# Kernel tuning notes

Measured on AMD Instinct MI355X. Metric: run time of the kernel, lower is better.

## Reference

```python
import jax, jax.numpy as jnp
import numpy as np

B, N, D, S, H, ITERS = 128, 4096, 64, 7, 128, 3
EPS = 1e-8
LN_EPS = 1e-5


def _ln(x, g, b):
    mu = jnp.mean(x, axis=-1, keepdims=True)
    var = jnp.mean(jnp.square(x - mu), axis=-1, keepdims=True)
    return (x - mu) * jax.lax.rsqrt(var + LN_EPS) * g + b


def setup_inputs() -> dict:
    key = jax.random.key(0)
    ks = jax.random.split(key, 20)
    xav = lambda k, shp: jax.random.normal(k, shp, jnp.float32) * (2.0 / sum(shp[-2:])) ** 0.5
    inp = {
        "inputs": jax.random.normal(ks[0], (B, N, D), jnp.float32),
        "noise_bg": jax.random.normal(ks[1], (B, 1, D), jnp.float32),
        "noise_fg": jax.random.normal(ks[2], (B, S - 1, D), jnp.float32),
        "ln_in_g": jnp.ones((D,), jnp.float32), "ln_in_b": jnp.zeros((D,), jnp.float32),
        "ln_slot_g": jnp.ones((D,), jnp.float32), "ln_slot_b": jnp.zeros((D,), jnp.float32),
        "ln_mlp_g": jnp.ones((D,), jnp.float32), "ln_mlp_b": jnp.zeros((D,), jnp.float32),
        "Wq": xav(ks[3], (D, D)), "Wk": xav(ks[4], (D, D)), "Wv": xav(ks[5], (D, D)),
        "W_ih": xav(ks[6], (3 * D, D)), "W_hh": xav(ks[7], (3 * D, D)),
        "b_ih": jnp.zeros((3 * D,), jnp.float32), "b_hh": jnp.zeros((3 * D,), jnp.float32),
        "mlp_w1": xav(ks[8], (H, D)), "mlp_b1": jnp.zeros((H,), jnp.float32),
        "mlp_w2": xav(ks[9], (D, H)), "mlp_b2": jnp.zeros((D,), jnp.float32),
        "slots_bg_mu": xav(ks[10], (1, 1, D)),
        "slots_bg_log_sigma": xav(ks[11], (1, 1, D)),
        "slots_mu": xav(ks[12], (1, 1, D)),
        "slots_log_sigma": xav(ks[13], (1, 1, D)),
    }
    return inp


def _gru(x, h, W_ih, W_hh, b_ih, b_hh):
    # x, h: [M, D]; PyTorch GRUCell math, gate order r, z, n
    gi = x @ W_ih.T + b_ih
    gh = h @ W_hh.T + b_hh
    i_r, i_z, i_n = jnp.split(gi, 3, axis=-1)
    h_r, h_z, h_n = jnp.split(gh, 3, axis=-1)
    r = jax.nn.sigmoid(i_r + h_r)
    z = jax.nn.sigmoid(i_z + h_z)
    n = jnp.tanh(i_n + r * h_n)
    return (1.0 - z) * n + z * h


def reference(inputs, noise_bg, noise_fg, ln_in_g, ln_in_b, ln_slot_g, ln_slot_b,
              ln_mlp_g, ln_mlp_b, Wq, Wk, Wv, W_ih, W_hh, b_ih, b_hh,
              mlp_w1, mlp_b1, mlp_w2, mlp_b2,
              slots_bg_mu, slots_bg_log_sigma, slots_mu, slots_log_sigma):
    x = _ln(inputs, ln_in_g, ln_in_b)          # [B, N, D]
    k = jnp.einsum('bnd,ed->bne', x, Wk)       # [B, N, D]
    v = jnp.einsum('bnd,ed->bne', x, Wv)

    bg = slots_bg_mu + jnp.exp(slots_bg_log_sigma) * noise_bg   # [B, 1, D]
    fg = slots_mu + jnp.exp(slots_log_sigma) * noise_fg          # [B, S-1, D]
    slots = jnp.concatenate([bg, fg], axis=1)                    # [B, S, D]

    scale = D ** (-0.5)
    for _ in range(ITERS):
        slots_prev = slots
        s = _ln(slots, ln_slot_g, ln_slot_b)
        q = jnp.einsum('bsd,ed->bse', s, Wq)                     # [B, S, D]
        logits = scale * jnp.einsum('bnd,bsd->bns', k, q)        # [B, N, S]
        attn = jax.nn.softmax(logits, axis=-1) + EPS             # softmax over slots
        attn = attn / jnp.sum(attn, axis=1, keepdims=True)       # renorm over inputs
        updates = jnp.einsum('bns,bnd->bsd', attn, v)            # [B, S, D]
        h = _gru(updates.reshape(B * S, D), slots_prev.reshape(B * S, D),
                 W_ih, W_hh, b_ih, b_hh).reshape(B, S, D)
        m = _ln(h, ln_mlp_g, ln_mlp_b)
        m = jax.nn.relu(m @ mlp_w1.T + mlp_b1) @ mlp_w2.T + mlp_b2
        slots = h + m
    return slots
```

## Files before the change

kernel.cpp:

```cpp
#include <hip/hip_runtime.h>

#define BB 128
#define NN 4096
#define DD 64
#define SS 7
#define HH 128
#define N_ITERS 3
#define EPS_ATTN 1e-8f
#define LN_EPS 1e-5f

typedef unsigned short ushortT;
using short8  = __attribute__((ext_vector_type(8))) short;
using floatx4 = __attribute__((ext_vector_type(4))) float;
using uint4v  = __attribute__((ext_vector_type(4))) unsigned;

__device__ __forceinline__ ushortT f2bf(float f) {
    unsigned x = __builtin_bit_cast(unsigned, f);
    x = x + 0x7fff + ((x >> 16) & 1);
    return (ushortT)(x >> 16);
}
__device__ __forceinline__ void wave_stats64(float x, float& mu, float& var) {
    float s1 = x, s2 = x * x;
#pragma unroll
    for (int off = 32; off > 0; off >>= 1) {
        s1 += __shfl_xor(s1, off);
        s2 += __shfl_xor(s2, off);
    }
    mu  = s1 * (1.f / 64.f);
    var = s2 * (1.f / 64.f) - mu * mu;
}

__global__ void prep_w(const float* __restrict__ Wih, const float* __restrict__ Whh,
                       const float* __restrict__ w1, const float* __restrict__ w2,
                       const float* __restrict__ Wv, const float* __restrict__ Wq,
                       const float* __restrict__ Wk,
                       float* __restrict__ WihT, float* __restrict__ WhhT,
                       float* __restrict__ w1T, float* __restrict__ w2T,
                       float* __restrict__ WvT, float* __restrict__ WqkT) {
    if (blockIdx.x >= 192) {
        int idx = (blockIdx.x - 192) * 256 + threadIdx.x;
        int d = idx >> 6, tt = idx & 63;
        float acc = 0.f;
#pragma unroll 8
        for (int e = 0; e < 64; ++e) acc += Wk[e * 64 + tt] * Wq[e * 64 + d];
        WqkT[d * 64 + tt] = 0.125f * acc;
        return;
    }
    int i = blockIdx.x * 256 + threadIdx.x;
    if (i < 12288) {
        int e = i >> 6, d = i & 63;
        WihT[d * 192 + e] = Wih[i];
    } else if (i < 24576) {
        int j = i - 12288; int e = j >> 6, d = j & 63;
        WhhT[d * 192 + e] = Whh[j];
    } else if (i < 32768) {
        int j = i - 24576; int e = j >> 6, d = j & 63;
        w1T[d * 128 + e] = w1[j];
    } else if (i < 40960) {
        int j = i - 32768; int e = j >> 7, h = j & 127;
        w2T[h * 64 + e] = w2[j];
    } else if (i < 45056) {
        int j = i - 40960; int d = j >> 6, e = j & 63;
        WvT[e * 64 + d] = Wv[j];
    }
}

__global__ __launch_bounds__(256) void attn_kernel(
    int first,
    const float* __restrict__ x,
    const float* __restrict__ lng, const float* __restrict__ lnb,
    ushortT* __restrict__ xnf,
    const ushortT* __restrict__ qk_bf,
    float* __restrict__ pxn_p, float* __restrict__ den_p) {
    int t = threadIdx.x;
    int ck = blockIdx.x, b = ck >> 5;
    int w = t >> 6, lane = t & 63, m = lane & 15, qd = lane >> 4;
    __shared__ __align__(16) ushortT xnT[64 * 140];
    __shared__ __align__(16) ushortT p_lds[16][136];

    short8 aq0 = {}, aq1 = {};
    if (m < 8) {
        const ushortT* qb = qk_bf + b * 512 + m * 64 + qd * 8;
        aq0 = *reinterpret_cast<const short8*>(qb);
        aq1 = *reinterpret_cast<const short8*>(qb + 32);
    }

    unsigned xw[2][8];
    if (first) {
        float4 g4[2][2], b4[2][2];
#pragma unroll
        for (int c = 0; c < 2; ++c) {
            g4[c][0] = *reinterpret_cast<const float4*>(lng + c * 32 + qd * 8);
            g4[c][1] = *reinterpret_cast<const float4*>(lng + c * 32 + qd * 8 + 4);
            b4[c][0] = *reinterpret_cast<const float4*>(lnb + c * 32 + qd * 8);
            b4[c][1] = *reinterpret_cast<const float4*>(lnb + c * 32 + qd * 8 + 4);
        }
#pragma unroll
        for (int tile = 0; tile < 2; ++tile) {
            long R = (long)ck * 128 + w * 32 + tile * 16 + m;
            float4 xa[2][2];
#pragma unroll
            for (int c = 0; c < 2; ++c) {
                xa[c][0] = *reinterpret_cast<const float4*>(x + R * 64 + c * 32 + qd * 8);
                xa[c][1] = *reinterpret_cast<const float4*>(x + R * 64 + c * 32 + qd * 8 + 4);
            }
            float s1 = 0.f, s2 = 0.f;
#pragma unroll
            for (int c = 0; c < 2; ++c)
#pragma unroll
                for (int h = 0; h < 2; ++h) {
                    float4 v = xa[c][h];
                    s1 += v.x + v.y + v.z + v.w;
                    s2 += v.x * v.x + v.y * v.y + v.z * v.z + v.w * v.w;
                }
            s1 += __shfl_xor(s1, 16); s2 += __shfl_xor(s2, 16);
            s1 += __shfl_xor(s1, 32); s2 += __shfl_xor(s2, 32);
            float mu = s1 * (1.f / 64.f);
            float var = s2 * (1.f / 64.f) - mu * mu;
            float rs = rsqrtf(var + LN_EPS);
#pragma unroll
            for (int c = 0; c < 2; ++c)
#pragma unroll
                for (int h = 0; h < 2; ++h) {
                    float n0 = (xa[c][h].x - mu) * rs * g4[c][h].x + b4[c][h].x;
                    float n1 = (xa[c][h].y - mu) * rs * g4[c][h].y + b4[c][h].y;
                    float n2 = (xa[c][h].z - mu) * rs * g4[c][h].z + b4[c][h].z;
                    float n3 = (xa[c][h].w - mu) * rs * g4[c][h].w + b4[c][h].w;
                    xw[tile][c * 4 + h * 2]     = (unsigned)f2bf(n0) | ((unsigned)f2bf(n1) << 16);
                    xw[tile][c * 4 + h * 2 + 1] = (unsigned)f2bf(n2) | ((unsigned)f2bf(n3) << 16);
                }
            ushortT* xp = xnf + (long)ck * 8192 + w * 2048 + tile * 1024 + lane * 16;
            *reinterpret_cast<uint4*>(xp) =
                make_uint4(xw[tile][0], xw[tile][1], xw[tile][2], xw[tile][3]);
            *reinterpret_cast<uint4*>(xp + 8) =
                make_uint4(xw[tile][4], xw[tile][5], xw[tile][6], xw[tile][7]);
        }
    } else {
#pragma unroll
        for (int tile = 0; tile < 2; ++tile) {
            const ushortT* xp = xnf + (long)ck * 8192 + w * 2048 + tile * 1024 + lane * 16;
            uint4 u0 = *reinterpret_cast<const uint4*>(xp);
            uint4 u1 = *reinterpret_cast<const uint4*>(xp + 8);
            xw[tile][0] = u0.x; xw[tile][1] = u0.y; xw[tile][2] = u0.z; xw[tile][3] = u0.w;
            xw[tile][4] = u1.x; xw[tile][5] = u1.y; xw[tile][6] = u1.z; xw[tile][7] = u1.w;
        }
    }

#pragma unroll
    for (int tile = 0; tile < 2; ++tile) {
        int Re = (w * 32 + tile * 16 + m) & ~1;
#pragma unroll
        for (int c = 0; c < 2; ++c) {
            unsigned pt[4];
#pragma unroll
            for (int k = 0; k < 4; ++k) pt[k] = __shfl_xor(xw[tile][c * 4 + k], 1);
#pragma unroll
            for (int kk = 0; kk < 2; ++kk) {
                unsigned own = (m & 1) ? xw[tile][c * 4 + 2 + kk] : xw[tile][c * 4 + kk];
                unsigned par = (m & 1) ? pt[2 + kk] : pt[kk];
                unsigned a   = (m & 1) ? par : own;
                unsigned bb  = (m & 1) ? own : par;
                unsigned lo = (a & 0xffffu) | (bb << 16);
                unsigned hi = (a >> 16)     | (bb & 0xffff0000u);
                int e = c * 32 + qd * 8 + 2 * kk + ((m & 1) ? 4 : 0);
                *reinterpret_cast<unsigned*>(&xnT[e * 140 + Re])       = lo;
                *reinterpret_cast<unsigned*>(&xnT[(e + 1) * 140 + Re]) = hi;
            }
        }
    }

    floatx4 accT0 = {0.f, 0.f, 0.f, 0.f}, accT1 = {0.f, 0.f, 0.f, 0.f};
    {
        uint4v b00 = {xw[0][0], xw[0][1], xw[0][2], xw[0][3]};
        uint4v b01 = {xw[0][4], xw[0][5], xw[0][6], xw[0][7]};
        accT0 = __builtin_amdgcn_mfma_f32_16x16x32_bf16(aq0,
                    __builtin_bit_cast(short8, b00), accT0, 0, 0, 0);
        accT0 = __builtin_amdgcn_mfma_f32_16x16x32_bf16(aq1,
                    __builtin_bit_cast(short8, b01), accT0, 0, 0, 0);
        uint4v b10 = {xw[1][0], xw[1][1], xw[1][2], xw[1][3]};
        uint4v b11 = {xw[1][4], xw[1][5], xw[1][6], xw[1][7]};
        accT1 = __builtin_amdgcn_mfma_f32_16x16x32_bf16(aq0,
                    __builtin_bit_cast(short8, b10), accT1, 0, 0, 0);
        accT1 = __builtin_amdgcn_mfma_f32_16x16x32_bf16(aq1,
                    __builtin_bit_cast(short8, b11), accT1, 0, 0, 0);
    }

    float lgA[4], lgB[4];
#pragma unroll
    for (int r = 0; r < 4; ++r) {
        float hi = __shfl_xor(accT1[r], 32);
        float wk = (qd < 2) ? accT0[r] : hi;
        float pr = __shfl_xor(wk, 16);
        lgA[r] = (qd & 1) ? pr : wk;
        lgB[r] = (qd & 1) ? wk : pr;
    }
    float mx = fmaxf(fmaxf(fmaxf(lgA[0], lgA[1]), fmaxf(lgA[2], lgA[3])),
                     fmaxf(fmaxf(lgB[0], lgB[1]), lgB[2]));
    float eA[4], eB[3], sum = 0.f;
#pragma unroll
    for (int r = 0; r < 4; ++r) { eA[r] = __expf(lgA[r] - mx); sum += eA[r]; }
#pragma unroll
    for (int r = 0; r < 3; ++r) { eB[r] = __expf(lgB[r] - mx); sum += eB[r]; }
    float inv = 1.f / sum;
    int prow = w * 32 + (qd >> 1) * 16 + m;
    if ((qd & 1) == 0) {
#pragma unroll
        for (int r = 0; r < 4; ++r) p_lds[r][prow] = f2bf(eA[r] * inv + EPS_ATTN);
    } else {
#pragma unroll
        for (int r = 0; r < 3; ++r) p_lds[4 + r][prow] = f2bf(eB[r] * inv + EPS_ATTN);
    }
    __syncthreads();

    short8 ones;
#pragma unroll
    for (int j = 0; j < 8; ++j) ones[j] = (short)0x3F80;

    floatx4 acc2 = {0.f, 0.f, 0.f, 0.f}, accd = {0.f, 0.f, 0.f, 0.f};
#pragma unroll
    for (int ks = 0; ks < 4; ++ks) {
        short8 ap = *reinterpret_cast<const short8*>(&p_lds[m][ks * 32 + qd * 8]);
        const ushortT* xp = xnT + (w * 16 + m) * 140 + ks * 32 + qd * 8;
        uint2 u0 = *reinterpret_cast<const uint2*>(xp);
        uint2 u1 = *reinterpret_cast<const uint2*>(xp + 4);
        uint4v bb = {u0.x, u0.y, u1.x, u1.y};
        acc2 = __builtin_amdgcn_mfma_f32_16x16x32_bf16(ap,
                   __builtin_bit_cast(short8, bb), acc2, 0, 0, 0);
        accd = __builtin_amdgcn_mfma_f32_16x16x32_bf16(ap, ones, accd, 0, 0, 0);
    }
#pragma unroll
    for (int r = 0; r < 4; ++r) {
        int s = qd * 4 + r;
        if (s < 7) pxn_p[((long)ck * 7 + s) * 64 + w * 16 + m] = acc2[r];
    }
    if (w == 0 && m == 0) {
#pragma unroll
        for (int r = 0; r < 4; ++r) {
            int s = qd * 4 + r;
            if (s < 7) den_p[ck * 8 + s] = accd[r];
        }
    }
}

__global__ __launch_bounds__(192) void slot_update_q(
    int mode,
    const float* __restrict__ pxn_p, const float* __restrict__ den_p,
    float* __restrict__ slots,
    const float* __restrict__ nbg, const float* __restrict__ nfg,
    const float* __restrict__ bgmu, const float* __restrict__ bgls,
    const float* __restrict__ fmu, const float* __restrict__ fls,
    const float* __restrict__ WihT, const float* __restrict__ WhhT,
    const float* __restrict__ bih, const float* __restrict__ bhh,
    const float* __restrict__ lng, const float* __restrict__ lnb,
    const float* __restrict__ w1T, const float* __restrict__ b1,
    const float* __restrict__ w2T, const float* __restrict__ b2,
    const float* __restrict__ WvT, const float* __restrict__ WqkT,
    const float* __restrict__ sg, const float* __restrict__ sb,
    ushortT* __restrict__ qk_bf, float* __restrict__ outp) {
    int bs = blockIdx.x, t = threadIdx.x;
    int b = bs / 7, s = bs % 7;
    __shared__ float pxnL[64], hprevL[64], updL[64], giL[192], ghL[192],
                     mnL[64], m1L[128], xnL[64];
    __shared__ float denL;
    float res = 0.f;
    if (mode == 0) {
        if (t < 64) {
            if (s == 0) res = bgmu[t] + __expf(bgls[t]) * nbg[b * 64 + t];
            else        res = fmu[t]  + __expf(fls[t])  * nfg[(b * 6 + s - 1) * 64 + t];
        }
    } else {
        if (t < 64) {
            float psum = 0.f;
#pragma unroll 8
            for (int c = 0; c < 32; ++c)
                psum += pxn_p[((long)(b * 32 + c) * 7 + s) * 64 + t];
            pxnL[t] = psum;
        } else if (t < 96) {
            float dv = den_p[(b * 32 + (t - 64)) * 8 + s];
#pragma unroll
            for (int off = 16; off > 0; off >>= 1) dv += __shfl_xor(dv, off, 32);
            if (t == 64) denL = dv;
        } else if (t >= 128) {
            hprevL[t - 128] = slots[bs * 64 + (t - 128)];
        }
        __syncthreads();
        if (t < 64) {
            float nm = 0.f;
#pragma unroll 8
            for (int e = 0; e < 64; ++e) nm += pxnL[e] * WvT[e * 64 + t];
            updL[t] = nm / denL;
        }
        __syncthreads();
        {
            float a = bih[t], h2 = bhh[t];
#pragma unroll 8
            for (int d = 0; d < 64; ++d) {
                a  += updL[d]   * WihT[d * 192 + t];
                h2 += hprevL[d] * WhhT[d * 192 + t];
            }
            giL[t] = a; ghL[t] = h2;
        }
        __syncthreads();
        if (t < 64) {
            float r = 1.f / (1.f + __expf(-(giL[t] + ghL[t])));
            float z = 1.f / (1.f + __expf(-(giL[64 + t] + ghL[64 + t])));
            float n = tanhf(giL[128 + t] + r * ghL[128 + t]);
            float h = (1.f - z) * n + z * hprevL[t];
            res = h;
            float mu, var;
            wave_stats64(h, mu, var);
            mnL[t] = (h - mu) * rsqrtf(var + LN_EPS) * lng[t] + lnb[t];
        }
        __syncthreads();
        if (t < 128) {
            float a = b1[t];
#pragma unroll 8
            for (int d = 0; d < 64; ++d) a += mnL[d] * w1T[d * 128 + t];
            m1L[t] = fmaxf(a, 0.f);
        }
        __syncthreads();
        if (t < 64) {
            float a = b2[t];
#pragma unroll 8
            for (int h2 = 0; h2 < 128; ++h2) a += m1L[h2] * w2T[h2 * 64 + t];
            res += a;
        }
    }
    if (t < 64) slots[bs * 64 + t] = res;
    if (mode == 2) {
        if (t < 64) outp[bs * 64 + t] = res;
        return;
    }
    if (t < 64) {
        float mu, var;
        wave_stats64(res, mu, var);
        xnL[t] = (res - mu) * rsqrtf(var + LN_EPS) * sg[t] + sb[t];
    }
    __syncthreads();
    if (t < 64) {
        float qk = 0.f;
#pragma unroll 8
        for (int d = 0; d < 64; ++d) qk += xnL[d] * WqkT[d * 64 + t];
        qk_bf[b * 512 + s * 64 + t] = f2bf(qk);
        if (s == 0) qk_bf[b * 512 + 7 * 64 + t] = 0;
    }
}

extern "C" void kernel_launch(void* const* d_in, const int* in_sizes, int n_in,
                              void* d_out, int out_size, void* d_ws, size_t ws_size,
                              hipStream_t stream) {
    const float* inputs    = (const float*)d_in[0];
    const float* noise_bg  = (const float*)d_in[1];
    const float* noise_fg  = (const float*)d_in[2];
    const float* ln_in_g   = (const float*)d_in[3];
    const float* ln_in_b   = (const float*)d_in[4];
    const float* ln_slot_g = (const float*)d_in[5];
    const float* ln_slot_b = (const float*)d_in[6];
    const float* ln_mlp_g  = (const float*)d_in[7];
    const float* ln_mlp_b  = (const float*)d_in[8];
    const float* Wq        = (const float*)d_in[9];
    const float* Wk        = (const float*)d_in[10];
    const float* Wv        = (const float*)d_in[11];
    const float* W_ih      = (const float*)d_in[12];
    const float* W_hh      = (const float*)d_in[13];
    const float* b_ih      = (const float*)d_in[14];
    const float* b_hh      = (const float*)d_in[15];
    const float* mlp_w1    = (const float*)d_in[16];
    const float* mlp_b1    = (const float*)d_in[17];
    const float* mlp_w2    = (const float*)d_in[18];
    const float* mlp_b2    = (const float*)d_in[19];
    const float* sbg_mu    = (const float*)d_in[20];
    const float* sbg_ls    = (const float*)d_in[21];
    const float* s_mu      = (const float*)d_in[22];
    const float* s_ls      = (const float*)d_in[23];

    char* ws = (char*)d_ws;
    size_t off = 0;
    auto alloc = [&](size_t bytes) {
        void* p = ws + off;
        off += (bytes + 255) & ~(size_t)255;
        return p;
    };
    ushortT* xnf   = (ushortT*)alloc((size_t)BB * NN * 64 * 2);
    float* slots   = (float*)alloc(57344 * 4);
    ushortT* qk_bf = (ushortT*)alloc((size_t)BB * 512 * 2);
    float* pxn_p   = (float*)alloc((size_t)4096 * 7 * 64 * 4);
    float* den_p   = (float*)alloc(4096 * 8 * 4);
    float* WihT    = (float*)alloc(12288 * 4);
    float* WhhT    = (float*)alloc(12288 * 4);
    float* w1T     = (float*)alloc(8192 * 4);
    float* w2T     = (float*)alloc(8192 * 4);
    float* WvT     = (float*)alloc(4096 * 4);
    float* WqkT    = (float*)alloc(4096 * 4);
    if (off > ws_size) return;

    prep_w<<<208, 256, 0, stream>>>(W_ih, W_hh, mlp_w1, mlp_w2, Wv, Wq, Wk,
                                    WihT, WhhT, w1T, w2T, WvT, WqkT);
    slot_update_q<<<896, 192, 0, stream>>>(0, pxn_p, den_p, slots,
                                           noise_bg, noise_fg, sbg_mu, sbg_ls,
                                           s_mu, s_ls, WihT, WhhT, b_ih, b_hh,
                                           ln_mlp_g, ln_mlp_b, w1T, mlp_b1,
                                           w2T, mlp_b2, WvT, WqkT,
                                           ln_slot_g, ln_slot_b,
                                           qk_bf, (float*)d_out);
    for (int it = 0; it < N_ITERS; ++it) {
        attn_kernel<<<4096, 256, 0, stream>>>((it == 0) ? 1 : 0,
                                              inputs, ln_in_g, ln_in_b,
                                              xnf, qk_bf, pxn_p, den_p);
        slot_update_q<<<896, 192, 0, stream>>>((it == N_ITERS - 1) ? 2 : 1,
                                               pxn_p, den_p, slots,
                                               noise_bg, noise_fg, sbg_mu, sbg_ls,
                                               s_mu, s_ls, WihT, WhhT, b_ih, b_hh,
                                               ln_mlp_g, ln_mlp_b, w1T, mlp_b1,
                                               w2T, mlp_b2, WvT, WqkT,
                                               ln_slot_g, ln_slot_b,
                                               qk_bf, (float*)d_out);
    }
}
```

Measured before the change: 352.9 us.

## Fuse whole slot-attention pipeline into one cooperative persistent kernel

Replaces the eight-launch sequence (weight prep, slot init, and three attention plus slot-update rounds) with a single cooperative kernel of 1024 blocks that uses grid syncs between phases. Each block layer-normalises four 128-row chunks of the input once and keeps them in registers as bf16 across all three iterations, which removes the workspace round trip for the normalised inputs and the per-iteration reload. The intent is to cut launch gaps and memory traffic. In exchange it adds grid-wide barriers, higher register pressure from holding 64 packed words per thread, and a dependence on 4 blocks per CU being co-resident. It falls back to the old multi-kernel path if cooperative launch is unsupported or fails.

```diff
diff --git a/kernel.cpp b/kernel.cpp
--- a/kernel.cpp
+++ b/kernel.cpp
@@ -1,4 +1,6 @@
 #include <hip/hip_runtime.h>
+#include <hip/hip_cooperative_groups.h>
+namespace cg = cooperative_groups;
 
 #define BB 128
 #define NN 4096
@@ -28,6 +30,329 @@
     }
     mu  = s1 * (1.f / 64.f);
     var = s2 * (1.f / 64.f) - mu * mu;
+}
+
+__global__ __launch_bounds__(256, 4) void fused_all(
+    const float* __restrict__ x,
+    const float* __restrict__ lngi, const float* __restrict__ lnbi,
+    const float* __restrict__ Wih, const float* __restrict__ Whh,
+    const float* __restrict__ w1, const float* __restrict__ w2,
+    const float* __restrict__ Wv, const float* __restrict__ Wq,
+    const float* __restrict__ Wk,
+    float* __restrict__ WihT, float* __restrict__ WhhT,
+    float* __restrict__ w1T, float* __restrict__ w2T,
+    float* __restrict__ WvT, float* __restrict__ WqkT,
+    float* __restrict__ slots,
+    const float* __restrict__ nbg, const float* __restrict__ nfg,
+    const float* __restrict__ bgmu, const float* __restrict__ bgls,
+    const float* __restrict__ fmu, const float* __restrict__ fls,
+    const float* __restrict__ bih, const float* __restrict__ bhh,
+    const float* __restrict__ lnmg, const float* __restrict__ lnmb,
+    const float* __restrict__ b1, const float* __restrict__ b2,
+    const float* __restrict__ sg, const float* __restrict__ sb,
+    ushortT* __restrict__ qk_bf,
+    float* __restrict__ pxn_p, float* __restrict__ den_p,
+    float* __restrict__ outp) {
+    cg::grid_group gg = cg::this_grid();
+    int t = threadIdx.x, bid = blockIdx.x;
+    int w = t >> 6, lane = t & 63, m = lane & 15, qd = lane >> 4;
+    int bt = bid >> 3, cgrp = bid & 7;
+    bool act = bid < 896;
+    int b_s = bid / 7, s_s = bid % 7;
+
+    __shared__ __align__(16) ushortT xnT[64 * 140];
+    __shared__ __align__(16) ushortT p_lds[16][136];
+    __shared__ float pxnL[64], hprevL[64], updL[64], giL[192], ghL[192],
+                     mnL[64], m1L[128], xnL[64];
+    __shared__ float denL;
+
+    if (bid < 192) {
+        int i = bid * 256 + t;
+        if (i < 12288) {
+            int e = i >> 6, d = i & 63;
+            WihT[d * 192 + e] = Wih[i];
+        } else if (i < 24576) {
+            int j = i - 12288; int e = j >> 6, d = j & 63;
+            WhhT[d * 192 + e] = Whh[j];
+        } else if (i < 32768) {
+            int j = i - 24576; int e = j >> 6, d = j & 63;
+            w1T[d * 128 + e] = w1[j];
+        } else if (i < 40960) {
+            int j = i - 32768; int e = j >> 7, h = j & 127;
+            w2T[h * 64 + e] = w2[j];
+        } else if (i < 45056) {
+            int j = i - 40960; int d = j >> 6, e = j & 63;
+            WvT[e * 64 + d] = Wv[j];
+        }
+    } else if (bid < 208) {
+        int idx = (bid - 192) * 256 + t;
+        int d = idx >> 6, tt2 = idx & 63;
+        float acc = 0.f;
+#pragma unroll 8
+        for (int e = 0; e < 64; ++e) acc += Wk[e * 64 + tt2] * Wq[e * 64 + d];
+        WqkT[d * 64 + tt2] = 0.125f * acc;
+    }
+
+    unsigned xw[4][2][8];
+    {
+        float4 g4[2][2], h4[2][2];
+#pragma unroll
+        for (int c = 0; c < 2; ++c) {
+            g4[c][0] = *reinterpret_cast<const float4*>(lngi + c * 32 + qd * 8);
+            g4[c][1] = *reinterpret_cast<const float4*>(lngi + c * 32 + qd * 8 + 4);
+            h4[c][0] = *reinterpret_cast<const float4*>(lnbi + c * 32 + qd * 8);
+            h4[c][1] = *reinterpret_cast<const float4*>(lnbi + c * 32 + qd * 8 + 4);
+        }
+#pragma unroll
+        for (int c4 = 0; c4 < 4; ++c4)
+#pragma unroll
+            for (int tile = 0; tile < 2; ++tile) {
+                long R = ((long)bt * 32 + cgrp * 4 + c4) * 128 + w * 32 + tile * 16 + m;
+                float4 xa[2][2];
+#pragma unroll
+                for (int c = 0; c < 2; ++c) {
+                    xa[c][0] = *reinterpret_cast<const float4*>(x + R * 64 + c * 32 + qd * 8);
+                    xa[c][1] = *reinterpret_cast<const float4*>(x + R * 64 + c * 32 + qd * 8 + 4);
+                }
+                float s1 = 0.f, s2 = 0.f;
+#pragma unroll
+                for (int c = 0; c < 2; ++c)
+#pragma unroll
+                    for (int h = 0; h < 2; ++h) {
+                        float4 v = xa[c][h];
+                        s1 += v.x + v.y + v.z + v.w;
+                        s2 += v.x * v.x + v.y * v.y + v.z * v.z + v.w * v.w;
+                    }
+                s1 += __shfl_xor(s1, 16); s2 += __shfl_xor(s2, 16);
+                s1 += __shfl_xor(s1, 32); s2 += __shfl_xor(s2, 32);
+                float mu = s1 * (1.f / 64.f);
+                float var = s2 * (1.f / 64.f) - mu * mu;
+                float rs = rsqrtf(var + LN_EPS);
+#pragma unroll
+                for (int c = 0; c < 2; ++c)
+#pragma unroll
+                    for (int h = 0; h < 2; ++h) {
+                        float n0 = (xa[c][h].x - mu) * rs * g4[c][h].x + h4[c][h].x;
+                        float n1 = (xa[c][h].y - mu) * rs * g4[c][h].y + h4[c][h].y;
+                        float n2 = (xa[c][h].z - mu) * rs * g4[c][h].z + h4[c][h].z;
+                        float n3 = (xa[c][h].w - mu) * rs * g4[c][h].w + h4[c][h].w;
+                        xw[c4][tile][c * 4 + h * 2] =
+                            (unsigned)f2bf(n0) | ((unsigned)f2bf(n1) << 16);
+                        xw[c4][tile][c * 4 + h * 2 + 1] =
+                            (unsigned)f2bf(n2) | ((unsigned)f2bf(n3) << 16);
+                    }
+            }
+    }
+    __threadfence(); gg.sync(); __threadfence();
+
+    {
+        float res = 0.f;
+        if (act && t < 64) {
+            if (s_s == 0) res = bgmu[t] + __expf(bgls[t]) * nbg[b_s * 64 + t];
+            else          res = fmu[t]  + __expf(fls[t])  * nfg[(b_s * 6 + s_s - 1) * 64 + t];
+            slots[bid * 64 + t] = res;
+            float mu, var;
+            wave_stats64(res, mu, var);
+            xnL[t] = (res - mu) * rsqrtf(var + LN_EPS) * sg[t] + sb[t];
+        }
+        __syncthreads();
+        if (act && t < 64) {
+            float qk = 0.f;
+#pragma unroll 8
+            for (int d = 0; d < 64; ++d) qk += xnL[d] * WqkT[d * 64 + t];
+            qk_bf[b_s * 512 + s_s * 64 + t] = f2bf(qk);
+            if (s_s == 0) qk_bf[b_s * 512 + 7 * 64 + t] = 0;
+        }
+    }
+    __threadfence(); gg.sync(); __threadfence();
+
+    for (int it = 0; it < N_ITERS; ++it) {
+        short8 aq0 = {}, aq1 = {};
+        if (m < 8) {
+            const ushortT* qb = qk_bf + bt * 512 + m * 64 + qd * 8;
+            aq0 = *reinterpret_cast<const short8*>(qb);
+            aq1 = *reinterpret_cast<const short8*>(qb + 32);
+        }
+        short8 ones;
+#pragma unroll
+        for (int j = 0; j < 8; ++j) ones[j] = (short)0x3F80;
+        floatx4 acc2 = {0.f, 0.f, 0.f, 0.f}, accd = {0.f, 0.f, 0.f, 0.f};
+
+#pragma unroll
+        for (int c4 = 0; c4 < 4; ++c4) {
+            __syncthreads();
+#pragma unroll
+            for (int tile = 0; tile < 2; ++tile) {
+                int Re = (w * 32 + tile * 16 + m) & ~1;
+#pragma unroll
+                for (int c = 0; c < 2; ++c) {
+                    unsigned pt[4];
+#pragma unroll
+                    for (int k = 0; k < 4; ++k)
+                        pt[k] = __shfl_xor(xw[c4][tile][c * 4 + k], 1);
+#pragma unroll
+                    for (int kk = 0; kk < 2; ++kk) {
+                        unsigned own = (m & 1) ? xw[c4][tile][c * 4 + 2 + kk]
+                                               : xw[c4][tile][c * 4 + kk];
+                        unsigned par = (m & 1) ? pt[2 + kk] : pt[kk];
+                        unsigned a   = (m & 1) ? par : own;
+                        unsigned bo  = (m & 1) ? own : par;
+                        unsigned lo = (a & 0xffffu) | (bo << 16);
+                        unsigned hi = (a >> 16)     | (bo & 0xffff0000u);
+                        int e = c * 32 + qd * 8 + 2 * kk + ((m & 1) ? 4 : 0);
+                        *reinterpret_cast<unsigned*>(&xnT[e * 140 + Re])       = lo;
+                        *reinterpret_cast<unsigned*>(&xnT[(e + 1) * 140 + Re]) = hi;
+                    }
+                }
+            }
+            floatx4 accT0 = {0.f, 0.f, 0.f, 0.f}, accT1 = {0.f, 0.f, 0.f, 0.f};
+            {
+                uint4v b00 = {xw[c4][0][0], xw[c4][0][1], xw[c4][0][2], xw[c4][0][3]};
+                uint4v b01 = {xw[c4][0][4], xw[c4][0][5], xw[c4][0][6], xw[c4][0][7]};
+                accT0 = __builtin_amdgcn_mfma_f32_16x16x32_bf16(aq0,
+                            __builtin_bit_cast(short8, b00), accT0, 0, 0, 0);
+                accT0 = __builtin_amdgcn_mfma_f32_16x16x32_bf16(aq1,
+                            __builtin_bit_cast(short8, b01), accT0, 0, 0, 0);
+                uint4v b10 = {xw[c4][1][0], xw[c4][1][1], xw[c4][1][2], xw[c4][1][3]};
+                uint4v b11 = {xw[c4][1][4], xw[c4][1][5], xw[c4][1][6], xw[c4][1][7]};
+                accT1 = __builtin_amdgcn_mfma_f32_16x16x32_bf16(aq0,
+                            __builtin_bit_cast(short8, b10), accT1, 0, 0, 0);
+                accT1 = __builtin_amdgcn_mfma_f32_16x16x32_bf16(aq1,
+                            __builtin_bit_cast(short8, b11), accT1, 0, 0, 0);
+            }
+            float lgA[4], lgB[4];
+#pragma unroll
+            for (int r = 0; r < 4; ++r) {
+                float hi = __shfl_xor(accT1[r], 32);
+                float wk = (qd < 2) ? accT0[r] : hi;
+                float pr = __shfl_xor(wk, 16);
+                lgA[r] = (qd & 1) ? pr : wk;
+                lgB[r] = (qd & 1) ? wk : pr;
+            }
+            float mx = fmaxf(fmaxf(fmaxf(lgA[0], lgA[1]), fmaxf(lgA[2], lgA[3])),
+                             fmaxf(fmaxf(lgB[0], lgB[1]), lgB[2]));
+            float eA[4], eB[3], sum = 0.f;
+#pragma unroll
+            for (int r = 0; r < 4; ++r) { eA[r] = __expf(lgA[r] - mx); sum += eA[r]; }
+#pragma unroll
+            for (int r = 0; r < 3; ++r) { eB[r] = __expf(lgB[r] - mx); sum += eB[r]; }
+            float inv = 1.f / sum;
+            int prow = w * 32 + (qd >> 1) * 16 + m;
+            if ((qd & 1) == 0) {
+#pragma unroll
+                for (int r = 0; r < 4; ++r) p_lds[r][prow] = f2bf(eA[r] * inv + EPS_ATTN);
+            } else {
+#pragma unroll
+                for (int r = 0; r < 3; ++r) p_lds[4 + r][prow] = f2bf(eB[r] * inv + EPS_ATTN);
+            }
+            __syncthreads();
+#pragma unroll
+            for (int ks = 0; ks < 4; ++ks) {
+                short8 ap = *reinterpret_cast<const short8*>(&p_lds[m][ks * 32 + qd * 8]);
+                const ushortT* xp = xnT + (w * 16 + m) * 140 + ks * 32 + qd * 8;
+                uint2 u0 = *reinterpret_cast<const uint2*>(xp);
+                uint2 u1 = *reinterpret_cast<const uint2*>(xp + 4);
+                uint4v bbv = {u0.x, u0.y, u1.x, u1.y};
+                acc2 = __builtin_amdgcn_mfma_f32_16x16x32_bf16(ap,
+                           __builtin_bit_cast(short8, bbv), acc2, 0, 0, 0);
+                accd = __builtin_amdgcn_mfma_f32_16x16x32_bf16(ap, ones, accd, 0, 0, 0);
+            }
+        }
+#pragma unroll
+        for (int r = 0; r < 4; ++r) {
+            int s = qd * 4 + r;
+            if (s < 7) pxn_p[((long)bid * 7 + s) * 64 + w * 16 + m] = acc2[r];
+        }
+        if (w == 0 && m == 0) {
+#pragma unroll
+            for (int r = 0; r < 4; ++r) {
+                int s = qd * 4 + r;
+                if (s < 7) den_p[bid * 8 + s] = accd[r];
+            }
+        }
+        __threadfence(); gg.sync(); __threadfence();
+
+        if (act) {
+            if (t < 64) {
+                float psum = 0.f;
+#pragma unroll
+                for (int k = 0; k < 8; ++k)
+                    psum += pxn_p[((long)(b_s * 8 + k) * 7 + s_s) * 64 + t];
+                pxnL[t] = psum;
+            } else if (t < 96) {
+                int l = t - 64;
+                float dv = (l < 8) ? den_p[(b_s * 8 + l) * 8 + s_s] : 0.f;
+                dv += __shfl_xor(dv, 4, 8);
+                dv += __shfl_xor(dv, 2, 8);
+                dv += __shfl_xor(dv, 1, 8);
+                if (l == 0) denL = dv;
+            } else if (t >= 128 && t < 192) {
+                hprevL[t - 128] = slots[bid * 64 + (t - 128)];
+            }
+        }
+        __syncthreads();
+        if (act && t < 64) {
+            float nm = 0.f;
+#pragma unroll 8
+            for (int e = 0; e < 64; ++e) nm += pxnL[e] * WvT[e * 64 + t];
+            updL[t] = nm / denL;
+        }
+        __syncthreads();
+        if (act && t < 192) {
+            float a = bih[t], h2 = bhh[t];
+#pragma unroll 8
+            for (int d = 0; d < 64; ++d) {
+                a  += updL[d]   * WihT[d * 192 + t];
+                h2 += hprevL[d] * WhhT[d * 192 + t];
+            }
+            giL[t] = a; ghL[t] = h2;
+        }
+        __syncthreads();
+        float res = 0.f;
+        if (act && t < 64) {
+            float r = 1.f / (1.f + __expf(-(giL[t] + ghL[t])));
+            float z = 1.f / (1.f + __expf(-(giL[64 + t] + ghL[64 + t])));
+            float n = tanhf(giL[128 + t] + r * ghL[128 + t]);
+            float h = (1.f - z) * n + z * hprevL[t];
+            res = h;
+            float mu, var;
+            wave_stats64(h, mu, var);
+            mnL[t] = (h - mu) * rsqrtf(var + LN_EPS) * lnmg[t] + lnmb[t];
+        }
+        __syncthreads();
+        if (act && t < 128) {
+            float a = b1[t];
+#pragma unroll 8
+            for (int d = 0; d < 64; ++d) a += mnL[d] * w1T[d * 128 + t];
+            m1L[t] = fmaxf(a, 0.f);
+        }
+        __syncthreads();
+        if (act && t < 64) {
+            float a = b2[t];
+#pragma unroll 8
+            for (int h2 = 0; h2 < 128; ++h2) a += m1L[h2] * w2T[h2 * 64 + t];
+            res += a;
+            slots[bid * 64 + t] = res;
+        }
+        if (it == N_ITERS - 1) {
+            if (act && t < 64) outp[bid * 64 + t] = res;
+        } else {
+            if (act && t < 64) {
+                float mu, var;
+                wave_stats64(res, mu, var);
+                xnL[t] = (res - mu) * rsqrtf(var + LN_EPS) * sg[t] + sb[t];
+            }
+            __syncthreads();
+            if (act && t < 64) {
+                float qk = 0.f;
+#pragma unroll 8
+                for (int d = 0; d < 64; ++d) qk += xnL[d] * WqkT[d * 64 + t];
+                qk_bf[b_s * 512 + s_s * 64 + t] = f2bf(qk);
+                if (s_s == 0) qk_bf[b_s * 512 + 7 * 64 + t] = 0;
+            }
+            __threadfence(); gg.sync(); __threadfence();
+        }
+    }
 }
 
 __global__ void prep_w(const float* __restrict__ Wih, const float* __restrict__ Whh,
@@ -84,7 +409,6 @@
         aq0 = *reinterpret_cast<const short8*>(qb);
         aq1 = *reinterpret_cast<const short8*>(qb + 32);
     }
-
     unsigned xw[2][8];
     if (first) {
         float4 g4[2][2], b4[2][2];
@@ -145,7 +469,6 @@
             xw[tile][4] = u1.x; xw[tile][5] = u1.y; xw[tile][6] = u1.z; xw[tile][7] = u1.w;
         }
     }
-
 #pragma unroll
     for (int tile = 0; tile < 2; ++tile) {
         int Re = (w * 32 + tile * 16 + m) & ~1;
@@ -168,7 +491,6 @@
             }
         }
     }
-
     floatx4 accT0 = {0.f, 0.f, 0.f, 0.f}, accT1 = {0.f, 0.f, 0.f, 0.f};
     {
         uint4v b00 = {xw[0][0], xw[0][1], xw[0][2], xw[0][3]};
@@ -184,7 +506,6 @@
         accT1 = __builtin_amdgcn_mfma_f32_16x16x32_bf16(aq1,
                     __builtin_bit_cast(short8, b11), accT1, 0, 0, 0);
     }
-
     float lgA[4], lgB[4];
 #pragma unroll
     for (int r = 0; r < 4; ++r) {
@@ -211,11 +532,9 @@
         for (int r = 0; r < 3; ++r) p_lds[4 + r][prow] = f2bf(eB[r] * inv + EPS_ATTN);
     }
     __syncthreads();
-
     short8 ones;
 #pragma unroll
     for (int j = 0; j < 8; ++j) ones[j] = (short)0x3F80;
-
     floatx4 acc2 = {0.f, 0.f, 0.f, 0.f}, accd = {0.f, 0.f, 0.f, 0.f};
 #pragma unroll
     for (int ks = 0; ks < 4; ++ks) {
@@ -393,6 +712,39 @@
     float* WvT     = (float*)alloc(4096 * 4);
     float* WqkT    = (float*)alloc(4096 * 4);
     if (off > ws_size) return;
+    float* outp = (float*)d_out;
+
+    static int coop_ok = -1;
+    if (coop_ok < 0) {
+        int dev = 0, v = 0;
+        hipGetDevice(&dev);
+        hipDeviceGetAttribute(&v, hipDeviceAttributeCooperativeLaunch, dev);
+        coop_ok = v;
+    }
+    if (coop_ok) {
+        void* args[] = {
+            (void*)&inputs, (void*)&ln_in_g, (void*)&ln_in_b,
+            (void*)&W_ih, (void*)&W_hh, (void*)&mlp_w1, (void*)&mlp_w2,
+            (void*)&Wv, (void*)&Wq, (void*)&Wk,
+            (void*)&WihT, (void*)&WhhT, (void*)&w1T, (void*)&w2T,
+            (void*)&WvT, (void*)&WqkT,
+            (void*)&slots,
+            (void*)&noise_bg, (void*)&noise_fg, (void*)&sbg_mu, (void*)&sbg_ls,
+            (void*)&s_mu, (void*)&s_ls,
+            (void*)&b_ih, (void*)&b_hh,
+            (void*)&ln_mlp_g, (void*)&ln_mlp_b,
+            (void*)&mlp_b1, (void*)&mlp_b2,
+            (void*)&ln_slot_g, (void*)&ln_slot_b,
+            (void*)&qk_bf,
+            (void*)&pxn_p, (void*)&den_p,
+            (void*)&outp
+        };
+        hipError_t e = hipLaunchCooperativeKernel((const void*)fused_all,
+                                                  dim3(1024), dim3(256),
+                                                  args, 0, stream);
+        if (e == hipSuccess) return;
+        coop_ok = 0;
+    }
 
     prep_w<<<208, 256, 0, stream>>>(W_ih, W_hh, mlp_w1, mlp_w2, Wv, Wq, Wk,
                                     WihT, WhhT, w1T, w2T, WvT, WqkT);
@@ -402,7 +754,7 @@
                                            ln_mlp_g, ln_mlp_b, w1T, mlp_b1,
                                            w2T, mlp_b2, WvT, WqkT,
                                            ln_slot_g, ln_slot_b,
-                                           qk_bf, (float*)d_out);
+                                           qk_bf, outp);
     for (int it = 0; it < N_ITERS; ++it) {
         attn_kernel<<<4096, 256, 0, stream>>>((it == 0) ? 1 : 0,
                                               inputs, ln_in_g, ln_in_b,
@@ -414,6 +766,6 @@
                                                ln_mlp_g, ln_mlp_b, w1T, mlp_b1,
                                                w2T, mlp_b2, WvT, WqkT,
                                                ln_slot_g, ln_slot_b,
-                                               qk_bf, (float*)d_out);
+                                               qk_bf, outp);
     }
 }
```

New measurement: 352.4 us. Within noise of the previous version (-0.1%).
